# Performance work log

Hardware: AMD Instinct MI355X
Metric: run time of the kernel (lower is better)

The kernel has to match this reference:

```python
import jax, jax.numpy as jnp
import numpy as np

N = 4096
IN_F = 256
H = 4
D = 64
WIN = 128
HALF = WIN // 2
TAU = 0.5
TOP_K = 32


def setup_inputs() -> dict:
    key = jax.random.key(0)
    ks = jax.random.split(key, 5)
    node_features = jax.random.normal(ks[0], (N, IN_F), dtype=jnp.float32)
    s = 1.0 / np.sqrt(IN_F)
    Wq = jax.random.normal(ks[1], (IN_F, H * D), dtype=jnp.float32) * s
    bq = jax.random.normal(ks[2], (H * D,), dtype=jnp.float32) * 0.01
    Wk = jax.random.normal(ks[3], (IN_F, H * D), dtype=jnp.float32) * s
    bk = jax.random.normal(ks[4], (H * D,), dtype=jnp.float32) * 0.01
    num_nodes_per_graph = jnp.full((8,), 512, dtype=jnp.int32)  # 8 graphs x 512 = N
    return {"node_features": node_features, "Wq": Wq, "bq": bq, "Wk": Wk,
            "bk": bk, "num_nodes_per_graph": num_nodes_per_graph, "num_relation": 1}


def reference(node_features, Wq, bq, Wk, bk, num_nodes_per_graph, num_relation):
    n = node_features.shape[0]
    scale = jnp.sqrt(jnp.asarray(D, node_features.dtype))

    Q = (node_features @ Wq + bq).reshape(n, H, D)
    K = (node_features @ Wk + bk).reshape(n, H, D)

    # segment boundaries (graph.num_nodes.repeat(num_relation) -> cumsum -> searchsorted)
    segment = jnp.tile(num_nodes_per_graph, num_relation)
    cum = jnp.cumsum(segment)
    i = jnp.arange(n)
    pos = jnp.searchsorted(cum, i, side='right')
    seg_start = jnp.where(pos == 0, 0, cum[jnp.maximum(pos - 1, 0)])
    seg_end = cum[jnp.minimum(pos, cum.shape[0] - 1)]

    start = jnp.maximum(seg_start, i - HALF)  # [N]
    end = jnp.minimum(seg_end, i + HALF)      # [N]

    gather_idx = start[:, None] + jnp.arange(WIN)[None, :]
    valid = gather_idx < end[:, None]
    gi = jnp.clip(gather_idx, 0, n - 1)
    Kw = jnp.where(valid[:, :, None, None], K[gi], 0.0)

    # scores over full window incl. zero padding (faithful: original does not mask softmax)
    scores = jnp.einsum('nhd,nmhd->nhm', Q, Kw) / scale / TAU
    attn = jax.nn.softmax(scores, axis=-1).mean(axis=1)

    # scatter attention rows into dense N x N (padded slots add 0)
    output = jnp.zeros((n, n), node_features.dtype).at[i[:, None], gi].add(
        jnp.where(valid, attn, 0.0))

    # gumbel_softmax_top_k(output, tau, hard=self.k) -> hard=True (k truthy)
    g = jax.random.gumbel(jax.random.key(42), output.shape, output.dtype)
    y_soft = jax.nn.softmax((output + g) / TAU, axis=-1)
    topk_idx = jax.lax.top_k(output, TOP_K)[1]                  # [N, TOP_K]
    y_hard = jnp.zeros_like(output).at[i[:, None], topk_idx].set(1.0)
    y = jax.lax.stop_gradient(y_hard - y_soft) + y_soft
    return y
```

## Files before the change

kernel.cpp:

```cpp
#include <hip/hip_runtime.h>

#define NF    256
#define HD    256
#define NH    4
#define DH    64
#define WINS  128
#define HALFW 64
#define TOPK  32
#define NB    4
#define GROWS 32

__device__ __forceinline__ float readlane_f(float v, int l) {
    return __uint_as_float(__builtin_amdgcn_readlane(__float_as_uint(v), l));
}
__device__ __forceinline__ float getc(const float4& v, int j) {
    return j == 0 ? v.x : j == 1 ? v.y : j == 2 ? v.z : v.w;
}

__global__ __launch_bounds__(256) void qk_gemm_kernel(
    const float* __restrict__ X,
    const float* __restrict__ Wq, const float* __restrict__ bq,
    const float* __restrict__ Wk, const float* __restrict__ bk,
    float* __restrict__ Qb, float* __restrict__ Kt, int n)
{
    const int t    = threadIdx.x;
    const int wave = t >> 6;
    const int lane = t & 63;
    const bool isK = (blockIdx.y != 0);
    const float* W   = isK ? Wk : Wq;
    const float* bia = isK ? bk : bq;

    const int r0  = blockIdx.x * GROWS + wave * 8;
    const int r0s = __builtin_amdgcn_readfirstlane(r0);
    const float* X0 = X + (size_t)r0s * NF;

    float4 acc[8];
#pragma unroll
    for (int rr = 0; rr < 8; ++rr) acc[rr] = make_float4(0.f, 0.f, 0.f, 0.f);

    for (int k = 0; k < NF; k += 8) {
        float4 wv[8];
#pragma unroll
        for (int u = 0; u < 8; ++u)
            wv[u] = *(const float4*)(W + (size_t)(k + u) * HD + 4 * lane);
#pragma unroll
        for (int u = 0; u < 8; ++u) {
#pragma unroll
            for (int rr = 0; rr < 8; ++rr) {
                float xk = X0[rr * NF + k + u];
                acc[rr].x += xk * wv[u].x;
                acc[rr].y += xk * wv[u].y;
                acc[rr].z += xk * wv[u].z;
                acc[rr].w += xk * wv[u].w;
            }
        }
    }

    const float4 bv = *(const float4*)(bia + 4 * lane);
#pragma unroll
    for (int rr = 0; rr < 8; ++rr) {
        acc[rr].x += bv.x; acc[rr].y += bv.y; acc[rr].z += bv.z; acc[rr].w += bv.w;
    }

    if (!isK) {
#pragma unroll
        for (int rr = 0; rr < 8; ++rr)
            *(float4*)(Qb + (size_t)(r0 + rr) * HD + 4 * lane) = acc[rr];
    } else {
#pragma unroll
        for (int j = 0; j < 4; ++j) {
            int col = 4 * lane + j;
            float4 lo = make_float4(getc(acc[0], j), getc(acc[1], j),
                                    getc(acc[2], j), getc(acc[3], j));
            float4 hi = make_float4(getc(acc[4], j), getc(acc[5], j),
                                    getc(acc[6], j), getc(acc[7], j));
            *(float4*)(Kt + (size_t)col * n + r0)     = lo;
            *(float4*)(Kt + (size_t)col * n + r0 + 4) = hi;
        }
    }
}

__global__ __launch_bounds__(256) void fill_zero_kernel(float4* __restrict__ p, int n4)
{
    int idx = blockIdx.x * 256 + threadIdx.x;
    int stride = gridDim.x * 256;
    float4 z = make_float4(0.f, 0.f, 0.f, 0.f);
    for (int c = idx; c < n4; c += stride) p[c] = z;
}

__global__ __launch_bounds__(256) void attn_topk_kernel(
    const float* __restrict__ Q,
    const float* __restrict__ KT,
    const int* __restrict__ nnpg, int n_graphs,
    const int* __restrict__ nrel,
    float* __restrict__ out, int n)
{
    const int t    = threadIdx.x;
    const int wave = t >> 6;
    const int lane = t & 63;
    const int i0   = blockIdx.x * NB;

    __shared__ float pslab[NH][NB][WINS];
    __shared__ float attnv[NB][WINS];

    int st[NB], en[NB];
    {
        int R = nrel[0];
        int total = n_graphs * R;
#pragma unroll
        for (int nn = 0; nn < NB; ++nn) {
            int i = i0 + nn, ss = 0, se = n, cum = 0;
            for (int e = 0; e < total; ++e) {
                int sz = nnpg[e % n_graphs];
                int nc = cum + sz;
                if (i < nc) { ss = cum; se = nc; break; }
                cum = nc;
            }
            st[nn] = max(ss, i - HALFW);
            en[nn] = min(se, i + HALFW);
        }
    }
    const int u0 = (min(min(st[0], st[1]), min(st[2], st[3]))) & ~3;
    const int Ue = max(max(en[0], en[1]), max(en[2], en[3]));
    const int U  = Ue - u0;

    float qreg[NB];
#pragma unroll
    for (int nn = 0; nn < NB; ++nn)
        qreg[nn] = Q[(size_t)(i0 + nn) * HD + wave * DH + lane];

    float4 acc[NB];
#pragma unroll
    for (int nn = 0; nn < NB; ++nn) acc[nn] = make_float4(0.f, 0.f, 0.f, 0.f);

    const bool act = (4 * lane < U);
    const float* kb = KT + (size_t)(wave * DH) * n + u0 + 4 * lane;

    for (int d0 = 0; d0 < DH; d0 += 8) {
        float4 kv[8];
#pragma unroll
        for (int u = 0; u < 8; ++u)
            kv[u] = act ? *(const float4*)(kb + (size_t)(d0 + u) * n)
                        : make_float4(0.f, 0.f, 0.f, 0.f);
#pragma unroll
        for (int u = 0; u < 8; ++u) {
#pragma unroll
            for (int nn = 0; nn < NB; ++nn) {
                float qd = readlane_f(qreg[nn], d0 + u);
                acc[nn].x += qd * kv[u].x;
                acc[nn].y += qd * kv[u].y;
                acc[nn].z += qd * kv[u].z;
                acc[nn].w += qd * kv[u].w;
            }
        }
    }

#pragma unroll
    for (int nn = 0; nn < NB; ++nn) {
        const int rs  = st[nn] - u0;
        const int re  = en[nn] - u0;
        const int win = en[nn] - st[nn];
        float s[4]; bool v[4];
#pragma unroll
        for (int j = 0; j < 4; ++j) {
            int c = 4 * lane + j;
            v[j] = (c >= rs) && (c < re);
            s[j] = getc(acc[nn], j) * 0.25f;
        }
        float lm = -1e30f;
#pragma unroll
        for (int j = 0; j < 4; ++j) if (v[j]) lm = fmaxf(lm, s[j]);
#pragma unroll
        for (int off = 32; off > 0; off >>= 1) lm = fmaxf(lm, __shfl_xor(lm, off));
        if (win < WINS) lm = fmaxf(lm, 0.f);
        float p[4], ls = 0.f;
#pragma unroll
        for (int j = 0; j < 4; ++j) {
            p[j] = v[j] ? expf(s[j] - lm) : 0.f;
            ls += p[j];
        }
#pragma unroll
        for (int off = 32; off > 0; off >>= 1) ls += __shfl_xor(ls, off);
        ls += (float)(WINS - win) * expf(-lm);
        float inv = 1.f / ls;
#pragma unroll
        for (int j = 0; j < 4; ++j) {
            int c = 4 * lane + j;
            if (v[j]) pslab[wave][nn][c - rs] = p[j] * inv;
        }
    }
    __syncthreads();

    {
        const int nn = wave;
        int stn = st[0], enn = en[0];
        if (nn == 1) { stn = st[1]; enn = en[1]; }
        if (nn == 2) { stn = st[2]; enn = en[2]; }
        if (nn == 3) { stn = st[3]; enn = en[3]; }
        const int win = enn - stn;

        float a0 = (lane < win)
            ? 0.25f * (pslab[0][nn][lane] + pslab[1][nn][lane] +
                       pslab[2][nn][lane] + pslab[3][nn][lane]) : -1.0f;
        float a1 = (lane + 64 < win)
            ? 0.25f * (pslab[0][nn][lane + 64] + pslab[1][nn][lane + 64] +
                       pslab[2][nn][lane + 64] + pslab[3][nn][lane + 64]) : -1.0f;
        attnv[nn][lane]      = a0;
        attnv[nn][lane + 64] = a1;
    }
    __syncthreads();

    {
        const int nn = wave;
        int stn = st[0], enn = en[0];
        if (nn == 1) { stn = st[1]; enn = en[1]; }
        if (nn == 2) { stn = st[2]; enn = en[2]; }
        if (nn == 3) { stn = st[3]; enn = en[3]; }
        const int win = enn - stn;

        const float w0v = attnv[nn][lane];
        const float w1v = attnv[nn][lane + 64];
        const int s0 = lane, s1 = lane + 64;
        int cnt0 = 0, cnt1 = 0;
#pragma unroll
        for (int j4 = 0; j4 < WINS / 4; ++j4) {
            float4 a4 = *(const float4*)&attnv[nn][j4 * 4];
            int jb = j4 * 4;
            cnt0 += (a4.x > w0v) || (a4.x == w0v && (jb + 0) < s0);
            cnt0 += (a4.y > w0v) || (a4.y == w0v && (jb + 1) < s0);
            cnt0 += (a4.z > w0v) || (a4.z == w0v && (jb + 2) < s0);
            cnt0 += (a4.w > w0v) || (a4.w == w0v && (jb + 3) < s0);
            cnt1 += (a4.x > w1v) || (a4.x == w1v && (jb + 0) < s1);
            cnt1 += (a4.y > w1v) || (a4.y == w1v && (jb + 1) < s1);
            cnt1 += (a4.z > w1v) || (a4.z == w1v && (jb + 2) < s1);
            cnt1 += (a4.w > w1v) || (a4.w == w1v && (jb + 3) < s1);
        }
        float* orow = out + (size_t)(i0 + nn) * n;
        if (s0 < win && cnt0 < TOPK) orow[stn + s0] = 1.0f;
        if (s1 < win && cnt1 < TOPK) orow[stn + s1] = 1.0f;
    }
}

extern "C" void kernel_launch(void* const* d_in, const int* in_sizes, int n_in,
                              void* d_out, int out_size, void* d_ws, size_t ws_size,
                              hipStream_t stream)
{
    const float* X  = (const float*)d_in[0];
    const float* Wq = (const float*)d_in[1];
    const float* bq = (const float*)d_in[2];
    const float* Wk = (const float*)d_in[3];
    const float* bk = (const float*)d_in[4];
    const int* nnpg = (const int*)d_in[5];
    const int* nrel = (const int*)d_in[6];

    const int n = in_sizes[0] / NF;
    const int n_graphs = in_sizes[5];

    float* Kt = (float*)d_ws;
    float* Qb = Kt + (size_t)n * HD;
    float* out = (float*)d_out;

    dim3 gg(n / GROWS, 2);
    qk_gemm_kernel<<<gg, 256, 0, stream>>>(X, Wq, bq, Wk, bk, Qb, Kt, n);

    fill_zero_kernel<<<2048, 256, 0, stream>>>((float4*)out, out_size >> 2);

    attn_topk_kernel<<<n / NB, 256, 0, stream>>>(Qb, Kt, nnpg, n_graphs, nrel, out, n);
}
```

Measured before the change: 154.5 us.

## Stage weight chunks in double-buffered LDS for QK GEMM and halve rows per block

The Q/K projection GEMM now stages 16-row chunks of the weight matrix in double-buffered shared memory with register prefetch. Each wave computes 4 rows instead of 8, which doubles the grid and reads X as float4. This is meant to cut redundant global weight loads and raise occupancy, at the cost of block-wide barriers and less reuse per weight fetch. Separately, the zero-fill launches twice as many blocks, and the segment search no longer breaks early, so the loop becomes branch-uniform but always scans every segment.

```diff
diff --git a/kernel.cpp b/kernel.cpp
--- a/kernel.cpp
+++ b/kernel.cpp
@@ -7,8 +7,10 @@
 #define WINS  128
 #define HALFW 64
 #define TOPK  32
+#define GROWS 16
+#define KCH   16
+#define NCH   (NF / KCH)
 #define NB    4
-#define GROWS 32
 
 __device__ __forceinline__ float readlane_f(float v, int l) {
     return __uint_as_float(__builtin_amdgcn_readlane(__float_as_uint(v), l));
@@ -23,6 +25,7 @@
     const float* __restrict__ Wk, const float* __restrict__ bk,
     float* __restrict__ Qb, float* __restrict__ Kt, int n)
 {
+    __shared__ float lw[2][KCH][HD];
     const int t    = threadIdx.x;
     const int wave = t >> 6;
     const int lane = t & 63;
@@ -30,52 +33,70 @@
     const float* W   = isK ? Wk : Wq;
     const float* bia = isK ? bk : bq;
 
-    const int r0  = blockIdx.x * GROWS + wave * 8;
-    const int r0s = __builtin_amdgcn_readfirstlane(r0);
-    const float* X0 = X + (size_t)r0s * NF;
-
-    float4 acc[8];
-#pragma unroll
-    for (int rr = 0; rr < 8; ++rr) acc[rr] = make_float4(0.f, 0.f, 0.f, 0.f);
-
-    for (int k = 0; k < NF; k += 8) {
-        float4 wv[8];
-#pragma unroll
-        for (int u = 0; u < 8; ++u)
-            wv[u] = *(const float4*)(W + (size_t)(k + u) * HD + 4 * lane);
-#pragma unroll
-        for (int u = 0; u < 8; ++u) {
-#pragma unroll
-            for (int rr = 0; rr < 8; ++rr) {
-                float xk = X0[rr * NF + k + u];
-                acc[rr].x += xk * wv[u].x;
-                acc[rr].y += xk * wv[u].y;
-                acc[rr].z += xk * wv[u].z;
-                acc[rr].w += xk * wv[u].w;
+    const int r0 = blockIdx.x * GROWS + wave * 4;
+    const float* Xw = X + (size_t)r0 * NF;
+
+    float4 acc[4];
+#pragma unroll
+    for (int r = 0; r < 4; ++r) acc[r] = make_float4(0.f, 0.f, 0.f, 0.f);
+
+    {
+        const float4* wsrc = (const float4*)W;
+        float4* dst = (float4*)&lw[0][0][0];
+#pragma unroll
+        for (int j = 0; j < 4; ++j) dst[j * 256 + t] = wsrc[j * 256 + t];
+    }
+
+    for (int c = 0; c < NCH; ++c) {
+        float4 pf[4];
+        const bool more = (c + 1 < NCH);
+        if (more) {
+            const float4* wsrc = (const float4*)(W + (size_t)(c + 1) * KCH * HD);
+#pragma unroll
+            for (int j = 0; j < 4; ++j) pf[j] = wsrc[j * 256 + t];
+        }
+        __syncthreads();
+        const float (*lwc)[HD] = lw[c & 1];
+
+#pragma unroll
+        for (int kk = 0; kk < KCH; kk += 4) {
+            float4 wv0 = *(const float4*)&lwc[kk + 0][4 * lane];
+            float4 wv1 = *(const float4*)&lwc[kk + 1][4 * lane];
+            float4 wv2 = *(const float4*)&lwc[kk + 2][4 * lane];
+            float4 wv3 = *(const float4*)&lwc[kk + 3][4 * lane];
+#pragma unroll
+            for (int r = 0; r < 4; ++r) {
+                float4 xv = *(const float4*)(Xw + r * NF + c * KCH + kk);
+                acc[r].x += xv.x * wv0.x + xv.y * wv1.x + xv.z * wv2.x + xv.w * wv3.x;
+                acc[r].y += xv.x * wv0.y + xv.y * wv1.y + xv.z * wv2.y + xv.w * wv3.y;
+                acc[r].z += xv.x * wv0.z + xv.y * wv1.z + xv.z * wv2.z + xv.w * wv3.z;
+                acc[r].w += xv.x * wv0.w + xv.y * wv1.w + xv.z * wv2.w + xv.w * wv3.w;
             }
         }
+        if (more) {
+            float4* dst = (float4*)&lw[(c + 1) & 1][0][0];
+#pragma unroll
+            for (int j = 0; j < 4; ++j) dst[j * 256 + t] = pf[j];
+        }
     }
 
     const float4 bv = *(const float4*)(bia + 4 * lane);
 #pragma unroll
-    for (int rr = 0; rr < 8; ++rr) {
-        acc[rr].x += bv.x; acc[rr].y += bv.y; acc[rr].z += bv.z; acc[rr].w += bv.w;
+    for (int r = 0; r < 4; ++r) {
+        acc[r].x += bv.x; acc[r].y += bv.y; acc[r].z += bv.z; acc[r].w += bv.w;
     }
 
     if (!isK) {
 #pragma unroll
-        for (int rr = 0; rr < 8; ++rr)
-            *(float4*)(Qb + (size_t)(r0 + rr) * HD + 4 * lane) = acc[rr];
+        for (int r = 0; r < 4; ++r)
+            *(float4*)(Qb + (size_t)(r0 + r) * HD + 4 * lane) = acc[r];
     } else {
 #pragma unroll
         for (int j = 0; j < 4; ++j) {
             int col = 4 * lane + j;
-            float4 lo = make_float4(getc(acc[0], j), getc(acc[1], j),
-                                    getc(acc[2], j), getc(acc[3], j));
-            float4 hi = make_float4(getc(acc[4], j), getc(acc[5], j),
-                                    getc(acc[6], j), getc(acc[7], j));
-            *(float4*)(Kt + (size_t)col * n + r0)     = lo;
-            *(float4*)(Kt + (size_t)col * n + r0 + 4) = hi;
+            *(float4*)(Kt + (size_t)col * n + r0) =
+                make_float4(getc(acc[0], j), getc(acc[1], j),
+                            getc(acc[2], j), getc(acc[3], j));
         }
     }
 }
@@ -113,7 +134,7 @@
             for (int e = 0; e < total; ++e) {
                 int sz = nnpg[e % n_graphs];
                 int nc = cum + sz;
-                if (i < nc) { ss = cum; se = nc; break; }
+                if (i >= cum && i < nc) { ss = cum; se = nc; }
                 cum = nc;
             }
             st[nn] = max(ss, i - HALFW);
@@ -263,7 +284,7 @@
     dim3 gg(n / GROWS, 2);
     qk_gemm_kernel<<<gg, 256, 0, stream>>>(X, Wq, bq, Wk, bk, Qb, Kt, n);
 
-    fill_zero_kernel<<<2048, 256, 0, stream>>>((float4*)out, out_size >> 2);
+    fill_zero_kernel<<<4096, 256, 0, stream>>>((float4*)out, out_size >> 2);
 
     attn_topk_kernel<<<n / NB, 256, 0, stream>>>(Qb, Kt, nnpg, n_graphs, nrel, out, n);
 }
```

Result: slower. 183.4 us (+18.7%).
